# Kernel optimization log

Measured on AMD Instinct MI355X. Metric: run time of the kernel, lower is better.

## Reference

```python
import jax, jax.numpy as jnp
import numpy as np

B, S, D, H = 2, 2048, 1024, 16
DH = D // H
SCALE = DH ** -0.5


def setup_inputs() -> dict:
    key = jax.random.key(0)
    ks = jax.random.split(key, 12)
    std = D ** -0.5
    return {
        "Q": jax.random.normal(ks[0], (B, S, D), jnp.float32),
        "K": jax.random.normal(ks[1], (B, S, D), jnp.float32),
        "V": jax.random.normal(ks[2], (B, S, D), jnp.float32),
        "mask": jnp.ones((B, S), jnp.int32),
        "Wq": jax.random.normal(ks[3], (D, D), jnp.float32) * std,
        "bq": jnp.zeros((D,), jnp.float32),
        "Wk": jax.random.normal(ks[4], (D, D), jnp.float32) * std,
        "bk": jnp.zeros((D,), jnp.float32),
        "Wv": jax.random.normal(ks[5], (D, D), jnp.float32) * std,
        "bv": jnp.zeros((D,), jnp.float32),
        "Wo": jax.random.normal(ks[6], (D, D), jnp.float32) * std,
        "bo": jnp.zeros((D,), jnp.float32),
    }


def reference(Q, K, V, mask, Wq, bq, Wk, bk, Wv, bv, Wo, bo):
    b, s, d = Q.shape
    # QKV projections (nn.Linear: x @ W.T + b), split into heads -> [b,h,s,dh]
    q = (Q @ Wq.T + bq).reshape(b, s, H, DH).transpose(0, 2, 1, 3)
    k = (K @ Wk.T + bk).reshape(b, s, H, DH).transpose(0, 2, 1, 3)
    v = (V @ Wv.T + bv).reshape(b, s, H, DH).transpose(0, 2, 1, 3)
    # full O(S^2) score matrix, as in the original (non-flash)
    scores = jnp.einsum("bhqd,bhkd->bhqk", q, k) * SCALE
    # padding mask: [b,1,1,s]
    scores = jnp.where(mask[:, None, None, :] == 0, -jnp.inf, scores)
    # causal mask (causal=True)
    causal = jnp.arange(s)[:, None] >= jnp.arange(s)[None, :]
    scores = jnp.where(causal[None, None], scores, -jnp.inf)
    attn = jax.nn.softmax(scores, axis=-1)
    out = jnp.einsum("bhqk,bhkd->bhqd", attn, v)
    out = out.transpose(0, 2, 1, 3).reshape(b, s, d)
    return out @ Wo.T + bo  # dropout p=0 -> identity
```

## Files before the change

### kernel.cpp

```cpp
#include <hip/hip_runtime.h>
#include <hip/hip_bf16.h>
#include <math.h>

#define Bc  2
#define Sc  2048
#define Dc  1024
#define Hc  16
#define DHc 64
#define SCALE 0.125f

typedef __attribute__((ext_vector_type(8))) short short8;
typedef __attribute__((ext_vector_type(4))) float f32x4;

__device__ inline f32x4 mfma16(short8 a, short8 b, f32x4 c) {
    return __builtin_amdgcn_mfma_f32_16x16x32_bf16(a, b, c, 0, 0, 0);
}

typedef __attribute__((address_space(1))) const unsigned int g_u32;
typedef __attribute__((address_space(3))) unsigned int l_u32;
__device__ inline void gld16(const void* g, void* l) {
    __builtin_amdgcn_global_load_lds((g_u32*)g, (l_u32*)l, 16, 0, 0);
}

__device__ inline short8 cvt8(float4 a, float4 b) {
    union { __hip_bfloat16 h[8]; short8 s; } u;
    u.h[0] = __float2bfloat16(a.x); u.h[1] = __float2bfloat16(a.y);
    u.h[2] = __float2bfloat16(a.z); u.h[3] = __float2bfloat16(a.w);
    u.h[4] = __float2bfloat16(b.x); u.h[5] = __float2bfloat16(b.y);
    u.h[6] = __float2bfloat16(b.z); u.h[7] = __float2bfloat16(b.w);
    return u.s;
}

__global__ __launch_bounds__(256) void castw_k(const float* __restrict__ W0, const float* __restrict__ W1,
                                               const float* __restrict__ W2, const float* __restrict__ W3,
                                               __hip_bfloat16* o0, __hip_bfloat16* o1,
                                               __hip_bfloat16* o2, __hip_bfloat16* o3)
{
    const float* s = blockIdx.y == 0 ? W0 : blockIdx.y == 1 ? W1 : blockIdx.y == 2 ? W2 : W3;
    __hip_bfloat16* d = blockIdx.y == 0 ? o0 : blockIdx.y == 1 ? o1 : blockIdx.y == 2 ? o2 : o3;
    size_t idx = ((size_t)blockIdx.x * 256 + threadIdx.x) * 8;
    float4 a = *(const float4*)(s + idx);
    float4 b = *(const float4*)(s + idx + 4);
    *(short8*)(d + idx) = cvt8(a, b);
}

__global__ __launch_bounds__(256, 2) void qkv_k(const float* __restrict__ Qi, const float* __restrict__ Ki,
                                                const float* __restrict__ Vi,
                                                const __hip_bfloat16* __restrict__ Wqb,
                                                const __hip_bfloat16* __restrict__ Wkb,
                                                const __hip_bfloat16* __restrict__ Wvb,
                                                const float* __restrict__ bq, const float* __restrict__ bk,
                                                const float* __restrict__ bv,
                                                __hip_bfloat16* __restrict__ qo, __hip_bfloat16* __restrict__ ko,
                                                __hip_bfloat16* __restrict__ vto)
{
    __shared__ __align__(16) __hip_bfloat16 As[2][128 * 64];
    __shared__ __align__(16) __hip_bfloat16 Bs[2][128 * 64];
    const int p   = blockIdx.x >> 8;
    const int blk = blockIdx.x & 255;
    const int bm  = blk & 31, bn = blk >> 5;
    const float* A = p == 0 ? Qi : p == 1 ? Ki : Vi;
    const __hip_bfloat16* W = p == 0 ? Wqb : p == 1 ? Wkb : Wvb;
    const float* bias = p == 0 ? bq : p == 1 ? bk : bv;

    const int tid = threadIdx.x, wave = tid >> 6, lane = tid & 63;
    const int quad = lane >> 4, l15 = lane & 15;
    const int wm = wave >> 1, wn = wave & 1;
    const int sw = l15 & 7;

    f32x4 acc[4][4] = {};
    float4 va[4][2];

#pragma unroll
    for (int i = 0; i < 4; ++i) {
        int c = wave * 64 + i * 256 + lane;
        int row = c >> 3, g = (c & 7) ^ (row & 7);
        gld16(W + (size_t)(bn * 128 + row) * 1024 + g * 8, (char*)&Bs[0][0] + (size_t)c * 16);
    }
#pragma unroll
    for (int i = 0; i < 4; ++i) {
        int c = tid + i * 256;
        int row = c >> 3, cc = c & 7, g = cc ^ (row & 7);
        const float* src = A + (size_t)(bm * 128 + row) * 1024 + g * 8;
        float4 v0 = *(const float4*)src;
        float4 v1 = *(const float4*)(src + 4);
        *(short8*)((char*)&As[0][0] + (size_t)row * 128 + cc * 16) = cvt8(v0, v1);
    }

    for (int kki = 0; kki < 16; ++kki) {
        const int buf = kki & 1;
        __syncthreads();
        if (kki < 15) {
            const int kk2 = (kki + 1) * 64;
#pragma unroll
            for (int i = 0; i < 4; ++i) {
                int c = wave * 64 + i * 256 + lane;
                int row = c >> 3, g = (c & 7) ^ (row & 7);
                gld16(W + (size_t)(bn * 128 + row) * 1024 + kk2 + g * 8,
                      (char*)&Bs[buf ^ 1][0] + (size_t)c * 16);
            }
#pragma unroll
            for (int i = 0; i < 4; ++i) {
                int c = tid + i * 256;
                int row = c >> 3, cc = c & 7, g = cc ^ (row & 7);
                const float* src = A + (size_t)(bm * 128 + row) * 1024 + kk2 + g * 8;
                va[i][0] = *(const float4*)src;
                va[i][1] = *(const float4*)(src + 4);
            }
        }

        short8 af[4][2], bf2[4][2];
#pragma unroll
        for (int mi = 0; mi < 4; ++mi)
#pragma unroll
            for (int h = 0; h < 2; ++h)
                af[mi][h] = *(const short8*)((char*)&As[buf][0] + (size_t)(wm * 64 + mi * 16 + l15) * 128 +
                                             ((((h << 2) + quad) ^ sw) << 4));
#pragma unroll
        for (int ni = 0; ni < 4; ++ni)
#pragma unroll
            for (int h = 0; h < 2; ++h)
                bf2[ni][h] = *(const short8*)((char*)&Bs[buf][0] + (size_t)(wn * 64 + ni * 16 + l15) * 128 +
                                              ((((h << 2) + quad) ^ sw) << 4));
#pragma unroll
        for (int mi = 0; mi < 4; ++mi)
#pragma unroll
            for (int ni = 0; ni < 4; ++ni) {
                acc[mi][ni] = mfma16(af[mi][0], bf2[ni][0], acc[mi][ni]);
                acc[mi][ni] = mfma16(af[mi][1], bf2[ni][1], acc[mi][ni]);
            }

        if (kki < 15) {
#pragma unroll
            for (int i = 0; i < 4; ++i) {
                int c = tid + i * 256;
                int row = c >> 3, cc = c & 7;
                *(short8*)((char*)&As[buf ^ 1][0] + (size_t)row * 128 + cc * 16) = cvt8(va[i][0], va[i][1]);
            }
        }
    }

    float bvv[4];
#pragma unroll
    for (int ni = 0; ni < 4; ++ni) bvv[ni] = bias[bn * 128 + wn * 64 + ni * 16 + l15];
#pragma unroll
    for (int mi = 0; mi < 4; ++mi) {
#pragma unroll
        for (int r = 0; r < 4; ++r) {
            int m = bm * 128 + wm * 64 + mi * 16 + quad * 4 + r;
            int b_ = m >> 11, s_ = m & 2047;
#pragma unroll
            for (int ni = 0; ni < 4; ++ni) {
                int n = bn * 128 + wn * 64 + ni * 16 + l15;
                int h_ = n >> 6, d_ = n & 63;
                float val = acc[mi][ni][r] + bvv[ni];
                if (p == 0) val *= SCALE;
                __hip_bfloat16 hv = __float2bfloat16(val);
                if (p < 2) {
                    __hip_bfloat16* dst = (p == 0 ? qo : ko);
                    dst[((size_t)(b_ * Hc + h_) * Sc + s_) * DHc + d_] = hv;
                } else {
                    int loc = s_ & 63;
                    int sp = (s_ & ~63) | ((loc & 15) << 2) | (loc >> 4);
                    vto[((size_t)(b_ * Hc + h_) * DHc + d_) * Sc + sp] = hv;
                }
            }
        }
    }
}

__global__ __launch_bounds__(256, 2) void attn_k(const __hip_bfloat16* __restrict__ qb,
                                                 const __hip_bfloat16* __restrict__ kb,
                                                 const __hip_bfloat16* __restrict__ vtb,
                                                 const int* __restrict__ mask,
                                                 __hip_bfloat16* __restrict__ ob)
{
    __shared__ __align__(16) __hip_bfloat16 Klds[2][64 * 64];
    __shared__ __align__(16) __hip_bfloat16 Vlds[2][64 * 64];
    __shared__ __align__(16) __hip_bfloat16 Plds[4][32 * 72];

    const int qt = 15 - (blockIdx.x >> 5);
    const int bh = blockIdx.x & 31;
    const int b  = bh >> 4;
    const int tid = threadIdx.x, wave = tid >> 6, lane = tid & 63;
    const int quad = lane >> 4, l15 = lane & 15;
    const int sw = l15 & 7;
    const int r0 = qt * 128 + wave * 32;

    const __hip_bfloat16* qh  = qb  + (size_t)bh * Sc * DHc;
    const __hip_bfloat16* kh  = kb  + (size_t)bh * Sc * DHc;
    const __hip_bfloat16* vth = vtb + (size_t)bh * DHc * Sc;

    short8 qf[2][2];
#pragma unroll
    for (int rc = 0; rc < 2; ++rc)
#pragma unroll
        for (int h = 0; h < 2; ++h)
            qf[rc][h] = *(const short8*)(qh + (size_t)(r0 + rc * 16 + l15) * DHc + h * 32 + quad * 8);

    f32x4 O[2][4] = {};
    float lsum[2][4] = {};

    const int nkt = 2 * qt + 2;

#pragma unroll
    for (int i = 0; i < 2; ++i) {
        int c = i * 256 + wave * 64 + lane;
        int row = c >> 3, g = (c & 7) ^ (row & 7);
        gld16(kh + (size_t)row * DHc + g * 8, (char*)&Klds[0][0] + (size_t)c * 16);
        gld16(vth + (size_t)row * Sc + g * 8, (char*)&Vlds[0][0] + (size_t)c * 16);
    }

    for (int kt = 0; kt < nkt; ++kt) {
        __syncthreads();
        if (kt + 1 < nkt) {
            const int kv1 = (kt + 1) * 64, nb = (kt + 1) & 1;
#pragma unroll
            for (int i = 0; i < 2; ++i) {
                int c = i * 256 + wave * 64 + lane;
                int row = c >> 3, g = (c & 7) ^ (row & 7);
                gld16(kh + (size_t)(kv1 + row) * DHc + g * 8, (char*)&Klds[nb][0] + (size_t)c * 16);
                gld16(vth + (size_t)row * Sc + kv1 + g * 8, (char*)&Vlds[nb][0] + (size_t)c * 16);
            }
        }
        const int kv0 = kt * 64, buf = kt & 1;
        if (kv0 >= r0 + 32) continue;

        f32x4 sc[2][4] = {};
#pragma unroll
        for (int h = 0; h < 2; ++h)
#pragma unroll
            for (int nc = 0; nc < 4; ++nc) {
                short8 kf = *(const short8*)((char*)&Klds[buf][0] +
                            (size_t)(nc * 16 + l15) * 128 + ((((h << 2) + quad) ^ sw) << 4));
                sc[0][nc] = mfma16(qf[0][h], kf, sc[0][nc]);
                sc[1][nc] = mfma16(qf[1][h], kf, sc[1][nc]);
            }

        float mb[4];
#pragma unroll
        for (int nc = 0; nc < 4; ++nc)
            mb[nc] = mask[b * Sc + kv0 + nc * 16 + l15] ? 0.f : -__builtin_inff();
        const bool notfull = (kv0 + 64 > r0);

#pragma unroll
        for (int rc = 0; rc < 2; ++rc)
#pragma unroll
            for (int r = 0; r < 4; ++r) {
                const int q_idx = r0 + rc * 16 + quad * 4 + r;
                float pv[4], ps = 0.f;
#pragma unroll
                for (int nc = 0; nc < 4; ++nc) {
                    float s = sc[rc][nc][r] + mb[nc];
                    if (notfull) {
                        int key = kv0 + nc * 16 + l15;
                        s = (key <= q_idx) ? s : -__builtin_inff();
                    }
                    s = fminf(s, 30.f);
                    pv[nc] = __expf(s);
                    ps += pv[nc];
                }
                lsum[rc][r] += ps;
                union { __hip_bfloat16 h[4]; unsigned long long u; } pp;
#pragma unroll
                for (int nc = 0; nc < 4; ++nc) pp.h[nc] = __float2bfloat16(pv[nc]);
                *(unsigned long long*)((char*)&Plds[wave][0] +
                    (size_t)(rc * 16 + quad * 4 + r) * 144 + l15 * 8) = pp.u;
            }

#pragma unroll
        for (int h = 0; h < 2; ++h) {
            short8 pf0 = *(const short8*)((char*)&Plds[wave][0] + (size_t)l15 * 144 + h * 64 + quad * 16);
            short8 pf1 = *(const short8*)((char*)&Plds[wave][0] + (size_t)(16 + l15) * 144 + h * 64 + quad * 16);
#pragma unroll
            for (int nc = 0; nc < 4; ++nc) {
                short8 vf = *(const short8*)((char*)&Vlds[buf][0] +
                            (size_t)(nc * 16 + l15) * 128 + ((((h << 2) + quad) ^ sw) << 4));
                O[0][nc] = mfma16(pf0, vf, O[0][nc]);
                O[1][nc] = mfma16(pf1, vf, O[1][nc]);
            }
        }
    }

#pragma unroll
    for (int rc = 0; rc < 2; ++rc)
#pragma unroll
        for (int r = 0; r < 4; ++r) {
            float l = lsum[rc][r];
#pragma unroll
            for (int off = 1; off < 16; off <<= 1) l += __shfl_xor(l, off);
            const float inv = 1.f / l;
            const int q_idx = r0 + rc * 16 + quad * 4 + r;
#pragma unroll
            for (int nc = 0; nc < 4; ++nc)
                ob[((size_t)bh * Sc + q_idx) * DHc + nc * 16 + l15] =
                    __float2bfloat16(O[rc][nc][r] * inv);
        }
}

__global__ __launch_bounds__(256, 2) void out_k(const __hip_bfloat16* __restrict__ Ab,
                                                const __hip_bfloat16* __restrict__ Wb,
                                                const float* __restrict__ bias,
                                                float* __restrict__ outp)
{
    __shared__ __align__(16) __hip_bfloat16 As[2][128 * 64];
    __shared__ __align__(16) __hip_bfloat16 Bs[2][64 * 64];
    const int bm = blockIdx.x & 31, bn = blockIdx.x >> 5;
    const int tid = threadIdx.x, wave = tid >> 6, lane = tid & 63;
    const int quad = lane >> 4, l15 = lane & 15;
    const int wm = wave >> 1, wn = wave & 1;
    const int sw = l15 & 7;

    f32x4 acc[4][2] = {};

#pragma unroll
    for (int i = 0; i < 4; ++i) {
        int c = wave * 64 + i * 256 + lane;
        int row = c >> 3, g = (c & 7) ^ (row & 7);
        int m = bm * 128 + row, b_ = m >> 11, s_ = m & 2047;
        gld16(Ab + (((size_t)(b_ * Hc) * Sc + s_) * DHc + g * 8), (char*)&As[0][0] + (size_t)c * 16);
    }
#pragma unroll
    for (int i = 0; i < 2; ++i) {
        int c = wave * 64 + i * 256 + lane;
        int row = c >> 3, g = (c & 7) ^ (row & 7);
        gld16(Wb + (size_t)(bn * 64 + row) * 1024 + g * 8, (char*)&Bs[0][0] + (size_t)c * 16);
    }

    for (int kki = 0; kki < 16; ++kki) {
        const int buf = kki & 1;
        __syncthreads();
        if (kki < 15) {
            const int h2 = kki + 1, kk2 = h2 * 64, nb = buf ^ 1;
#pragma unroll
            for (int i = 0; i < 4; ++i) {
                int c = wave * 64 + i * 256 + lane;
                int row = c >> 3, g = (c & 7) ^ (row & 7);
                int m = bm * 128 + row, b_ = m >> 11, s_ = m & 2047;
                gld16(Ab + (((size_t)(b_ * Hc + h2) * Sc + s_) * DHc + g * 8),
                      (char*)&As[nb][0] + (size_t)c * 16);
            }
#pragma unroll
            for (int i = 0; i < 2; ++i) {
                int c = wave * 64 + i * 256 + lane;
                int row = c >> 3, g = (c & 7) ^ (row & 7);
                gld16(Wb + (size_t)(bn * 64 + row) * 1024 + kk2 + g * 8,
                      (char*)&Bs[nb][0] + (size_t)c * 16);
            }
        }

        short8 af[4][2], bf2[2][2];
#pragma unroll
        for (int mi = 0; mi < 4; ++mi)
#pragma unroll
            for (int h = 0; h < 2; ++h)
                af[mi][h] = *(const short8*)((char*)&As[buf][0] + (size_t)(wm * 64 + mi * 16 + l15) * 128 +
                                             ((((h << 2) + quad) ^ sw) << 4));
#pragma unroll
        for (int ni = 0; ni < 2; ++ni)
#pragma unroll
            for (int h = 0; h < 2; ++h)
                bf2[ni][h] = *(const short8*)((char*)&Bs[buf][0] + (size_t)(wn * 32 + ni * 16 + l15) * 128 +
                                              ((((h << 2) + quad) ^ sw) << 4));
#pragma unroll
        for (int mi = 0; mi < 4; ++mi)
#pragma unroll
            for (int ni = 0; ni < 2; ++ni) {
                acc[mi][ni] = mfma16(af[mi][0], bf2[ni][0], acc[mi][ni]);
                acc[mi][ni] = mfma16(af[mi][1], bf2[ni][1], acc[mi][ni]);
            }
    }

    float bvv[2];
#pragma unroll
    for (int ni = 0; ni < 2; ++ni) bvv[ni] = bias[bn * 64 + wn * 32 + ni * 16 + l15];
#pragma unroll
    for (int mi = 0; mi < 4; ++mi)
#pragma unroll
        for (int r = 0; r < 4; ++r) {
            int m = bm * 128 + wm * 64 + mi * 16 + quad * 4 + r;
#pragma unroll
            for (int ni = 0; ni < 2; ++ni) {
                int n = bn * 64 + wn * 32 + ni * 16 + l15;
                outp[(size_t)m * 1024 + n] = acc[mi][ni][r] + bvv[ni];
            }
        }
}

extern "C" void kernel_launch(void* const* d_in, const int* in_sizes, int n_in,
                              void* d_out, int out_size, void* d_ws, size_t ws_size,
                              hipStream_t stream) {
    const float* Q   = (const float*)d_in[0];
    const float* K   = (const float*)d_in[1];
    const float* V   = (const float*)d_in[2];
    const int*  mask = (const int*)d_in[3];
    const float* Wq  = (const float*)d_in[4];
    const float* bq  = (const float*)d_in[5];
    const float* Wk  = (const float*)d_in[6];
    const float* bk  = (const float*)d_in[7];
    const float* Wv  = (const float*)d_in[8];
    const float* bv  = (const float*)d_in[9];
    const float* Wo  = (const float*)d_in[10];
    const float* bo  = (const float*)d_in[11];

    char* ws = (char*)d_ws;
    __hip_bfloat16* wqb = (__hip_bfloat16*)(ws);
    __hip_bfloat16* wkb = (__hip_bfloat16*)(ws + (2u << 20));
    __hip_bfloat16* wvb = (__hip_bfloat16*)(ws + (4u << 20));
    __hip_bfloat16* wob = (__hip_bfloat16*)(ws + (6u << 20));
    __hip_bfloat16* qbuf  = (__hip_bfloat16*)(ws + (8u << 20));
    __hip_bfloat16* kbuf  = (__hip_bfloat16*)(ws + (16u << 20));
    __hip_bfloat16* vtbuf = (__hip_bfloat16*)(ws + (24u << 20));

    castw_k<<<dim3(512, 4), 256, 0, stream>>>(Wq, Wk, Wv, Wo, wqb, wkb, wvb, wob);
    qkv_k<<<768, 256, 0, stream>>>(Q, K, V, wqb, wkb, wvb, bq, bk, bv, qbuf, kbuf, vtbuf);
    attn_k<<<512, 256, 0, stream>>>(qbuf, kbuf, vtbuf, mask, qbuf);
    out_k<<<512, 256, 0, stream>>>(qbuf, wob, bo, (float*)d_out);
}
```

Baseline: 243.5 us.

## Pre-cast Q/K/V to bf16 and single-buffer GEMM LDS for higher occupancy

The fp32 activations Q, K and V are now cast to bf16 in a separate pass that also casts the weights. This lets the QKV GEMM load both operands with direct global-to-LDS loads. The QKV and output projection GEMMs drop LDS double buffering and raise the launch-bounds occupancy target to 3 and 4 blocks per CU. They now rely on extra concurrent blocks to hide load latency, with an added barrier per k-step. The trade is an extra round trip of the activations through memory plus a second sync per iteration, in exchange for less LDS and register pressure and no in-loop conversion.

```diff
diff --git a/kernel.cpp b/kernel.cpp
--- a/kernel.cpp
+++ b/kernel.cpp
@@ -31,21 +31,36 @@
     return u.s;
 }
 
-__global__ __launch_bounds__(256) void castw_k(const float* __restrict__ W0, const float* __restrict__ W1,
-                                               const float* __restrict__ W2, const float* __restrict__ W3,
-                                               __hip_bfloat16* o0, __hip_bfloat16* o1,
-                                               __hip_bfloat16* o2, __hip_bfloat16* o3)
+__global__ __launch_bounds__(256) void castall_k(const float* __restrict__ W0, const float* __restrict__ W1,
+                                                 const float* __restrict__ W2, const float* __restrict__ W3,
+                                                 const float* __restrict__ I0, const float* __restrict__ I1,
+                                                 const float* __restrict__ I2,
+                                                 __hip_bfloat16* o0, __hip_bfloat16* o1,
+                                                 __hip_bfloat16* o2, __hip_bfloat16* o3,
+                                                 __hip_bfloat16* o4, __hip_bfloat16* o5,
+                                                 __hip_bfloat16* o6)
 {
-    const float* s = blockIdx.y == 0 ? W0 : blockIdx.y == 1 ? W1 : blockIdx.y == 2 ? W2 : W3;
-    __hip_bfloat16* d = blockIdx.y == 0 ? o0 : blockIdx.y == 1 ? o1 : blockIdx.y == 2 ? o2 : o3;
+    const int y = blockIdx.y;
+    const float* s; __hip_bfloat16* d; size_t n;
+    switch (y) {
+        case 0: s = W0; d = o0; n = 1u << 20; break;
+        case 1: s = W1; d = o1; n = 1u << 20; break;
+        case 2: s = W2; d = o2; n = 1u << 20; break;
+        case 3: s = W3; d = o3; n = 1u << 20; break;
+        case 4: s = I0; d = o4; n = 1u << 22; break;
+        case 5: s = I1; d = o5; n = 1u << 22; break;
+        default: s = I2; d = o6; n = 1u << 22; break;
+    }
     size_t idx = ((size_t)blockIdx.x * 256 + threadIdx.x) * 8;
+    if (idx >= n) return;
     float4 a = *(const float4*)(s + idx);
     float4 b = *(const float4*)(s + idx + 4);
     *(short8*)(d + idx) = cvt8(a, b);
 }
 
-__global__ __launch_bounds__(256, 2) void qkv_k(const float* __restrict__ Qi, const float* __restrict__ Ki,
-                                                const float* __restrict__ Vi,
+__global__ __launch_bounds__(256, 3) void qkv_k(const __hip_bfloat16* __restrict__ Qb,
+                                                const __hip_bfloat16* __restrict__ Kb,
+                                                const __hip_bfloat16* __restrict__ Vb,
                                                 const __hip_bfloat16* __restrict__ Wqb,
                                                 const __hip_bfloat16* __restrict__ Wkb,
                                                 const __hip_bfloat16* __restrict__ Wvb,
@@ -54,12 +69,12 @@
                                                 __hip_bfloat16* __restrict__ qo, __hip_bfloat16* __restrict__ ko,
                                                 __hip_bfloat16* __restrict__ vto)
 {
-    __shared__ __align__(16) __hip_bfloat16 As[2][128 * 64];
-    __shared__ __align__(16) __hip_bfloat16 Bs[2][128 * 64];
+    __shared__ __align__(16) __hip_bfloat16 As[128 * 64];
+    __shared__ __align__(16) __hip_bfloat16 Bs[128 * 64];
     const int p   = blockIdx.x >> 8;
     const int blk = blockIdx.x & 255;
     const int bm  = blk & 31, bn = blk >> 5;
-    const float* A = p == 0 ? Qi : p == 1 ? Ki : Vi;
+    const __hip_bfloat16* A = p == 0 ? Qb : p == 1 ? Kb : Vb;
     const __hip_bfloat16* W = p == 0 ? Wqb : p == 1 ? Wkb : Wvb;
     const float* bias = p == 0 ? bq : p == 1 ? bk : bv;
 
@@ -69,59 +84,45 @@
     const int sw = l15 & 7;
 
     f32x4 acc[4][4] = {};
-    float4 va[4][2];
 
 #pragma unroll
     for (int i = 0; i < 4; ++i) {
         int c = wave * 64 + i * 256 + lane;
         int row = c >> 3, g = (c & 7) ^ (row & 7);
-        gld16(W + (size_t)(bn * 128 + row) * 1024 + g * 8, (char*)&Bs[0][0] + (size_t)c * 16);
-    }
-#pragma unroll
-    for (int i = 0; i < 4; ++i) {
-        int c = tid + i * 256;
-        int row = c >> 3, cc = c & 7, g = cc ^ (row & 7);
-        const float* src = A + (size_t)(bm * 128 + row) * 1024 + g * 8;
-        float4 v0 = *(const float4*)src;
-        float4 v1 = *(const float4*)(src + 4);
-        *(short8*)((char*)&As[0][0] + (size_t)row * 128 + cc * 16) = cvt8(v0, v1);
+        gld16(A + (size_t)(bm * 128 + row) * 1024 + g * 8, (char*)As + (size_t)c * 16);
+        gld16(W + (size_t)(bn * 128 + row) * 1024 + g * 8, (char*)Bs + (size_t)c * 16);
     }
 
     for (int kki = 0; kki < 16; ++kki) {
-        const int buf = kki & 1;
         __syncthreads();
+
+        short8 af[4][2], bf2[4][2];
+#pragma unroll
+        for (int mi = 0; mi < 4; ++mi)
+#pragma unroll
+            for (int h = 0; h < 2; ++h)
+                af[mi][h] = *(const short8*)((char*)As + (size_t)(wm * 64 + mi * 16 + l15) * 128 +
+                                             ((((h << 2) + quad) ^ sw) << 4));
+#pragma unroll
+        for (int ni = 0; ni < 4; ++ni)
+#pragma unroll
+            for (int h = 0; h < 2; ++h)
+                bf2[ni][h] = *(const short8*)((char*)Bs + (size_t)(wn * 64 + ni * 16 + l15) * 128 +
+                                              ((((h << 2) + quad) ^ sw) << 4));
+
+        __syncthreads();
+
         if (kki < 15) {
             const int kk2 = (kki + 1) * 64;
 #pragma unroll
             for (int i = 0; i < 4; ++i) {
                 int c = wave * 64 + i * 256 + lane;
                 int row = c >> 3, g = (c & 7) ^ (row & 7);
-                gld16(W + (size_t)(bn * 128 + row) * 1024 + kk2 + g * 8,
-                      (char*)&Bs[buf ^ 1][0] + (size_t)c * 16);
-            }
-#pragma unroll
-            for (int i = 0; i < 4; ++i) {
-                int c = tid + i * 256;
-                int row = c >> 3, cc = c & 7, g = cc ^ (row & 7);
-                const float* src = A + (size_t)(bm * 128 + row) * 1024 + kk2 + g * 8;
-                va[i][0] = *(const float4*)src;
-                va[i][1] = *(const float4*)(src + 4);
-            }
-        }
-
-        short8 af[4][2], bf2[4][2];
-#pragma unroll
-        for (int mi = 0; mi < 4; ++mi)
-#pragma unroll
-            for (int h = 0; h < 2; ++h)
-                af[mi][h] = *(const short8*)((char*)&As[buf][0] + (size_t)(wm * 64 + mi * 16 + l15) * 128 +
-                                             ((((h << 2) + quad) ^ sw) << 4));
-#pragma unroll
-        for (int ni = 0; ni < 4; ++ni)
-#pragma unroll
-            for (int h = 0; h < 2; ++h)
-                bf2[ni][h] = *(const short8*)((char*)&Bs[buf][0] + (size_t)(wn * 64 + ni * 16 + l15) * 128 +
-                                              ((((h << 2) + quad) ^ sw) << 4));
+                gld16(A + (size_t)(bm * 128 + row) * 1024 + kk2 + g * 8, (char*)As + (size_t)c * 16);
+                gld16(W + (size_t)(bn * 128 + row) * 1024 + kk2 + g * 8, (char*)Bs + (size_t)c * 16);
+            }
+        }
+
 #pragma unroll
         for (int mi = 0; mi < 4; ++mi)
 #pragma unroll
@@ -129,15 +130,6 @@
                 acc[mi][ni] = mfma16(af[mi][0], bf2[ni][0], acc[mi][ni]);
                 acc[mi][ni] = mfma16(af[mi][1], bf2[ni][1], acc[mi][ni]);
             }
-
-        if (kki < 15) {
-#pragma unroll
-            for (int i = 0; i < 4; ++i) {
-                int c = tid + i * 256;
-                int row = c >> 3, cc = c & 7;
-                *(short8*)((char*)&As[buf ^ 1][0] + (size_t)row * 128 + cc * 16) = cvt8(va[i][0], va[i][1]);
-            }
-        }
     }
 
     float bvv[4];
@@ -298,13 +290,13 @@
         }
 }
 
-__global__ __launch_bounds__(256, 2) void out_k(const __hip_bfloat16* __restrict__ Ab,
+__global__ __launch_bounds__(256, 4) void out_k(const __hip_bfloat16* __restrict__ Ab,
                                                 const __hip_bfloat16* __restrict__ Wb,
                                                 const float* __restrict__ bias,
                                                 float* __restrict__ outp)
 {
-    __shared__ __align__(16) __hip_bfloat16 As[2][128 * 64];
-    __shared__ __align__(16) __hip_bfloat16 Bs[2][64 * 64];
+    __shared__ __align__(16) __hip_bfloat16 As[128 * 64];
+    __shared__ __align__(16) __hip_bfloat16 Bs[64 * 64];
     const int bm = blockIdx.x & 31, bn = blockIdx.x >> 5;
     const int tid = threadIdx.x, wave = tid >> 6, lane = tid & 63;
     const int quad = lane >> 4, l15 = lane & 15;
@@ -318,50 +310,51 @@
         int c = wave * 64 + i * 256 + lane;
         int row = c >> 3, g = (c & 7) ^ (row & 7);
         int m = bm * 128 + row, b_ = m >> 11, s_ = m & 2047;
-        gld16(Ab + (((size_t)(b_ * Hc) * Sc + s_) * DHc + g * 8), (char*)&As[0][0] + (size_t)c * 16);
+        gld16(Ab + (((size_t)(b_ * Hc) * Sc + s_) * DHc + g * 8), (char*)As + (size_t)c * 16);
     }
 #pragma unroll
     for (int i = 0; i < 2; ++i) {
         int c = wave * 64 + i * 256 + lane;
         int row = c >> 3, g = (c & 7) ^ (row & 7);
-        gld16(Wb + (size_t)(bn * 64 + row) * 1024 + g * 8, (char*)&Bs[0][0] + (size_t)c * 16);
+        gld16(Wb + (size_t)(bn * 64 + row) * 1024 + g * 8, (char*)Bs + (size_t)c * 16);
     }
 
     for (int kki = 0; kki < 16; ++kki) {
-        const int buf = kki & 1;
         __syncthreads();
+
+        short8 af[4][2], bf2[2][2];
+#pragma unroll
+        for (int mi = 0; mi < 4; ++mi)
+#pragma unroll
+            for (int h = 0; h < 2; ++h)
+                af[mi][h] = *(const short8*)((char*)As + (size_t)(wm * 64 + mi * 16 + l15) * 128 +
+                                             ((((h << 2) + quad) ^ sw) << 4));
+#pragma unroll
+        for (int ni = 0; ni < 2; ++ni)
+#pragma unroll
+            for (int h = 0; h < 2; ++h)
+                bf2[ni][h] = *(const short8*)((char*)Bs + (size_t)(wn * 32 + ni * 16 + l15) * 128 +
+                                              ((((h << 2) + quad) ^ sw) << 4));
+
+        __syncthreads();
+
         if (kki < 15) {
-            const int h2 = kki + 1, kk2 = h2 * 64, nb = buf ^ 1;
+            const int h2 = kki + 1, kk2 = h2 * 64;
 #pragma unroll
             for (int i = 0; i < 4; ++i) {
                 int c = wave * 64 + i * 256 + lane;
                 int row = c >> 3, g = (c & 7) ^ (row & 7);
                 int m = bm * 128 + row, b_ = m >> 11, s_ = m & 2047;
-                gld16(Ab + (((size_t)(b_ * Hc + h2) * Sc + s_) * DHc + g * 8),
-                      (char*)&As[nb][0] + (size_t)c * 16);
+                gld16(Ab + (((size_t)(b_ * Hc + h2) * Sc + s_) * DHc + g * 8), (char*)As + (size_t)c * 16);
             }
 #pragma unroll
             for (int i = 0; i < 2; ++i) {
                 int c = wave * 64 + i * 256 + lane;
                 int row = c >> 3, g = (c & 7) ^ (row & 7);
-                gld16(Wb + (size_t)(bn * 64 + row) * 1024 + kk2 + g * 8,
-                      (char*)&Bs[nb][0] + (size_t)c * 16);
-            }
-        }
-
-        short8 af[4][2], bf2[2][2];
-#pragma unroll
-        for (int mi = 0; mi < 4; ++mi)
-#pragma unroll
-            for (int h = 0; h < 2; ++h)
-                af[mi][h] = *(const short8*)((char*)&As[buf][0] + (size_t)(wm * 64 + mi * 16 + l15) * 128 +
-                                             ((((h << 2) + quad) ^ sw) << 4));
-#pragma unroll
-        for (int ni = 0; ni < 2; ++ni)
-#pragma unroll
-            for (int h = 0; h < 2; ++h)
-                bf2[ni][h] = *(const short8*)((char*)&Bs[buf][0] + (size_t)(wn * 32 + ni * 16 + l15) * 128 +
-                                              ((((h << 2) + quad) ^ sw) << 4));
+                gld16(Wb + (size_t)(bn * 64 + row) * 1024 + kk2 + g * 8, (char*)Bs + (size_t)c * 16);
+            }
+        }
+
 #pragma unroll
         for (int mi = 0; mi < 4; ++mi)
 #pragma unroll
@@ -411,9 +404,13 @@
     __hip_bfloat16* qbuf  = (__hip_bfloat16*)(ws + (8u << 20));
     __hip_bfloat16* kbuf  = (__hip_bfloat16*)(ws + (16u << 20));
     __hip_bfloat16* vtbuf = (__hip_bfloat16*)(ws + (24u << 20));
-
-    castw_k<<<dim3(512, 4), 256, 0, stream>>>(Wq, Wk, Wv, Wo, wqb, wkb, wvb, wob);
-    qkv_k<<<768, 256, 0, stream>>>(Q, K, V, wqb, wkb, wvb, bq, bk, bv, qbuf, kbuf, vtbuf);
+    __hip_bfloat16* Qbf   = (__hip_bfloat16*)(ws + (32u << 20));
+    __hip_bfloat16* Kbf   = (__hip_bfloat16*)(ws + (40u << 20));
+    __hip_bfloat16* Vbf   = (__hip_bfloat16*)(ws + (48u << 20));
+
+    castall_k<<<dim3(2048, 7), 256, 0, stream>>>(Wq, Wk, Wv, Wo, Q, K, V,
+                                                 wqb, wkb, wvb, wob, Qbf, Kbf, Vbf);
+    qkv_k<<<768, 256, 0, stream>>>(Qbf, Kbf, Vbf, wqb, wkb, wvb, bq, bk, bv, qbuf, kbuf, vtbuf);
     attn_k<<<512, 256, 0, stream>>>(qbuf, kbuf, vtbuf, mask, qbuf);
     out_k<<<512, 256, 0, stream>>>(qbuf, wob, bo, (float*)d_out);
 }
```

Result: faster. 230.6 us (-5.3%).
